# Kernel optimization log

Measured on AMD Instinct MI355X. Metric: run time of the kernel, lower is better.

## Reference

```python
import jax, jax.numpy as jnp
import numpy as np

NUM_ELECTRODES = 19
NUM_WINDOWS = 30
NUM_FREQS = 128
HEADS = 8
HID = 80
BATCH = 16
D_OUT = HEADS * HID  # 640


def _build_edge_index(num_nodes, num_windows):
    # spatiotemporal graph: dense intra-window blocks (incl. self-loops)
    # + bidirectional temporal edges between same electrode in adjacent windows
    srcs, dsts = [], []
    for w in range(num_windows):
        idx = np.arange(num_nodes) + w * num_nodes
        s, d = np.meshgrid(idx, idx, indexing='ij')
        srcs.append(s.ravel()); dsts.append(d.ravel())
    for w in range(num_windows - 1):
        a = np.arange(num_nodes) + w * num_nodes
        b = a + num_nodes
        srcs.append(a); dsts.append(b)
        srcs.append(b); dsts.append(a)
    return np.stack([np.concatenate(srcs), np.concatenate(dsts)]).astype(np.int32)


def setup_inputs() -> dict:
    key = jax.random.key(0)
    ks = jax.random.split(key, 12)
    f = NUM_FREQS
    x = jax.random.normal(ks[0], (BATCH, NUM_WINDOWS, NUM_FREQS, NUM_ELECTRODES), jnp.float32)
    s_in = 1.0 / np.sqrt(f)
    s_h = 1.0 / np.sqrt(D_OUT)
    Wl = jax.random.normal(ks[1], (D_OUT, f), jnp.float32) * s_in
    bl = jax.random.normal(ks[2], (D_OUT,), jnp.float32) * s_in
    Wr = jax.random.normal(ks[3], (D_OUT, f), jnp.float32) * s_in
    br = jax.random.normal(ks[4], (D_OUT,), jnp.float32) * s_in
    att = jax.random.normal(ks[5], (HEADS, HID), jnp.float32) * (1.0 / np.sqrt(HID))
    conv_bias = jax.random.normal(ks[6], (D_OUT,), jnp.float32) * 0.01
    Wpool = jax.random.normal(ks[7], (1, D_OUT), jnp.float32) * s_h
    bpool = jax.random.normal(ks[8], (1,), jnp.float32) * s_h
    Wfc = jax.random.normal(ks[9], (1, D_OUT), jnp.float32) * s_h
    bfc = jax.random.normal(ks[10], (1,), jnp.float32) * s_h
    edge_index = jnp.asarray(_build_edge_index(NUM_ELECTRODES, NUM_WINDOWS))
    return {"x": x, "edge_index": edge_index, "Wl": Wl, "bl": bl, "Wr": Wr, "br": br,
            "att": att, "conv_bias": conv_bias, "Wpool": Wpool, "bpool": bpool,
            "Wfc": Wfc, "bfc": bfc}


def reference(x, edge_index, Wl, bl, Wr, br, att, conv_bias, Wpool, bpool, Wfc, bfc):
    B, W, F, E19 = x.shape
    N = W * E19
    H, C = att.shape
    # (B, W, F, E) -> (B, W, E, F) -> (B, N, F)
    nodes = x.transpose(0, 1, 3, 2).reshape(B, N, F)
    src, dst = edge_index[0], edge_index[1]
    # GATv2: lin_l on source (messages), lin_r on target
    xl = (nodes @ Wl.T + bl).reshape(B, N, H, C)
    xr = (nodes @ Wr.T + br).reshape(B, N, H, C)
    msg = xl[:, src]                        # (B, E, H, C) source features
    key_feat = msg + xr[:, dst]             # (B, E, H, C)
    e = jnp.einsum('behc,hc->beh', jax.nn.leaky_relu(key_feat, 0.2), att)  # (B,E,H)

    def seg_softmax(e_b):  # (E, H), segment softmax over dst
        m = jax.ops.segment_max(e_b, dst, num_segments=N)
        ex = jnp.exp(e_b - m[dst])
        s = jax.ops.segment_sum(ex, dst, num_segments=N)
        return ex / (s[dst] + 1e-16)

    alpha = jax.vmap(seg_softmax)(e)        # (B, E, H)
    agg = jax.vmap(lambda m: jax.ops.segment_sum(m, dst, num_segments=N))(
        msg * alpha[..., None])             # (B, N, H, C)
    out = agg.reshape(B, N, H * C) + conv_bias
    out = jax.nn.elu(out)
    scores = out @ Wpool.T + bpool          # (B, N, 1)
    attn = jax.nn.softmax(scores, axis=1)
    pooled = (attn * out).sum(axis=1)       # (B, H*C)
    logits = pooled @ Wfc.T + bfc           # (B, 1)
    return logits.squeeze(1)
```

## Files before the change

kernel.cpp:

```cpp
#include <hip/hip_runtime.h>
#include <math.h>

#define B   16
#define NW  30
#define NE  19
#define NF  128
#define NH  8
#define NC  80
#define ND  640
#define NN  570
#define NROW (B*NN)

typedef _Float16 f16x2 __attribute__((ext_vector_type(2)));
typedef _Float16 f16x4 __attribute__((ext_vector_type(4)));
typedef _Float16 f16x8 __attribute__((ext_vector_type(8)));
typedef float    f32x16 __attribute__((ext_vector_type(16)));

#define WT_OFF   0
#define WT_SZ    (1280*128)
#define XL_OFF   (WT_OFF + WT_SZ)
#define XLR16_SZ (B*NN*ND/2)
#define XR_OFF   (XL_OFF + XLR16_SZ)
#define XT_OFF   (XR_OFF + XLR16_SZ)
#define SCP_OFF  (XT_OFF + 2*(NROW*NF/2))
#define SCP_SZ   (NH*B*NN)
#define QP_OFF   (SCP_OFF + SCP_SZ)

__global__ __launch_bounds__(256) void k0_prep(const float* __restrict__ Wl,
                                               const float* __restrict__ Wr,
                                               const float* __restrict__ x,
                                               _Float16* __restrict__ wph,
                                               _Float16* __restrict__ wpl,
                                               _Float16* __restrict__ xph,
                                               _Float16* __restrict__ xpl){
  int bx = blockIdx.x, t = threadIdx.x;
  if (bx < 160){
    int i = bx*256 + t;
    int dd = i >> 5, k = (i & 31) * 4;
    const float* srcp = (dd < 640) ? (Wl + dd*NF + k) : (Wr + (dd-640)*NF + k);
    float4 v = *(const float4*)srcp;
    _Float16 h0=(_Float16)v.x, h1=(_Float16)v.y, h2=(_Float16)v.z, h3=(_Float16)v.w;
    f16x4 hv = {h0, h1, h2, h3};
    f16x4 lv = {(_Float16)(v.x-(float)h0), (_Float16)(v.y-(float)h1),
                (_Float16)(v.z-(float)h2), (_Float16)(v.w-(float)h3)};
    int s = k >> 4, hh = (k >> 3) & 1, off = k & 7;
    size_t chunk = (((size_t)(dd >> 5)*8 + s)*64 + hh*32 + (dd & 31))*8 + off;
    *(f16x4*)(wph + chunk) = hv;
    *(f16x4*)(wpl + chunk) = lv;
    return;
  }
  int wb = bx - 160, w = wb % NW, b = wb / NW;
  __shared__ float ns[19*132];
  const float4* xs = (const float4*)(x + (size_t)((b*NW + w)*NF)*NE);
  for (int i = t; i < 608; i += 256){
    float4 v = xs[i];
    int idx = 4*i;
    float vv[4] = {v.x, v.y, v.z, v.w};
    #pragma unroll
    for (int k = 0; k < 4; ++k){
      int f = (idx + k) / NE, el = (idx + k) % NE;
      ns[el*132 + f] = vv[k];
    }
  }
  __syncthreads();
  for (int i = t; i < 608; i += 256){
    int el = i >> 5, k = (i & 31) * 4;
    float4 v = *(const float4*)&ns[el*132 + k];
    _Float16 h0=(_Float16)v.x, h1=(_Float16)v.y, h2=(_Float16)v.z, h3=(_Float16)v.w;
    f16x4 hv = {h0, h1, h2, h3};
    f16x4 lv = {(_Float16)(v.x-(float)h0), (_Float16)(v.y-(float)h1),
                (_Float16)(v.z-(float)h2), (_Float16)(v.w-(float)h3)};
    int n = (b*NW + w)*NE + el;
    int s = k >> 4, hh = (k >> 3) & 1, off = k & 7;
    size_t chunk = (((size_t)(n >> 5)*8 + s)*64 + hh*32 + (n & 31))*8 + off;
    *(f16x4*)(xph + chunk) = hv;
    *(f16x4*)(xpl + chunk) = lv;
  }
}

__global__ __launch_bounds__(256) void k1_gemm(const _Float16* __restrict__ xph,
                                               const _Float16* __restrict__ xpl,
                                               const _Float16* __restrict__ wph,
                                               const _Float16* __restrict__ wpl,
                                               const float* __restrict__ bl,
                                               const float* __restrict__ br,
                                               _Float16* __restrict__ xl,
                                               _Float16* __restrict__ xr){
  int t = threadIdx.x;
  int wave = t >> 6, lane = t & 63;
  int mt = blockIdx.x;
  int nt = blockIdx.y*4 + wave;

  __shared__ _Float16 ash[4096];
  __shared__ _Float16 asl[4096];
  {
    const f16x8* gh = (const f16x8*)(xph + (size_t)mt*4096);
    const f16x8* gl = (const f16x8*)(xpl + (size_t)mt*4096);
    f16x8* sh = (f16x8*)ash;
    f16x8* sl = (f16x8*)asl;
    #pragma unroll
    for (int c = 0; c < 2; ++c){
      sh[t + c*256] = gh[t + c*256];
      sl[t + c*256] = gl[t + c*256];
    }
  }
  __syncthreads();

  const f16x8* sah = (const f16x8*)ash + lane;
  const f16x8* sal = (const f16x8*)asl + lane;
  const f16x8* pbh = (const f16x8*)wph + (size_t)nt*8*64 + lane;
  const f16x8* pbl = (const f16x8*)wpl + (size_t)nt*8*64 + lane;

  f32x16 acc = {};
  #pragma unroll
  for (int s = 0; s < 8; ++s){
    f16x8 a_h = sah[s*64];
    f16x8 b_h = pbh[s*64];
    f16x8 a_l = sal[s*64];
    f16x8 b_l = pbl[s*64];
    acc = __builtin_amdgcn_mfma_f32_32x32x16_f16(a_h, b_h, acc, 0, 0, 0);
    acc = __builtin_amdgcn_mfma_f32_32x32x16_f16(a_l, b_h, acc, 0, 0, 0);
    acc = __builtin_amdgcn_mfma_f32_32x32x16_f16(a_h, b_l, acc, 0, 0, 0);
  }

  int bn = nt*32 + (lane & 31);
  float bias = (bn < 640) ? bl[bn] : br[bn - 640];
  _Float16* dstb = (bn < 640) ? xl : xr;
  int col = (bn < 640) ? bn : bn - 640;
  int rbase = mt*32 + 4*(lane >> 5);
  #pragma unroll
  for (int r = 0; r < 16; ++r){
    int node = rbase + (r & 3) + 8*(r >> 2);
    dstb[(size_t)node*ND + col] = (_Float16)(acc[r] + bias);
  }
}

__global__ __launch_bounds__(256, 4) void k2_gat(const _Float16* __restrict__ xl,
                                              const _Float16* __restrict__ xr,
                                              const float* __restrict__ att,
                                              const float* __restrict__ cb,
                                              const float* __restrict__ wpool,
                                              const float* __restrict__ wfc,
                                              float* __restrict__ scp,
                                              float* __restrict__ qp){
  int w = blockIdx.x, b = blockIdx.y, h = blockIdx.z, t = threadIdx.x;
  __shared__ _Float16 xl_s[57*88];
  __shared__ _Float16 xr_s[19*88];
  __shared__ _Float16 atth_s[80];
  __shared__ float cb_s[80], wp_s[80], wf_s[80];
  __shared__ float e_s[19*22];
  __shared__ float score_s[19], q_s[19];
  if (t < 19){ score_s[t] = 0.f; q_s[t] = 0.f; }
  const bool vp = (w > 0), vn = (w < NW-1);

  for (int i = t; i < 570; i += 256){
    int row = i / 10, c8 = i % 10;
    int node = -1;
    if (row < 19)        node = w*NE + row;
    else if (row < 38) { if (vp) node = (w-1)*NE + (row-19); }
    else               { if (vn) node = (w+1)*NE + (row-38); }
    if (node >= 0)
      *(f16x8*)&xl_s[row*88 + 8*c8] =
        *(const f16x8*)(xl + (size_t)(b*NN + node)*ND + h*80 + 8*c8);
  }
  for (int i = t; i < 190; i += 256){
    int row = i / 10, c8 = i % 10;
    int node = w*NE + row;
    *(f16x8*)&xr_s[row*88 + 8*c8] =
      *(const f16x8*)(xr + (size_t)(b*NN + node)*ND + h*80 + 8*c8);
  }
  if (t < 80){
    int a = t / 20, c4 = t % 20;
    if (a == 0){
      float4 v = *(const float4*)(att + h*80 + 4*c4);
      f16x4 hv = {(_Float16)v.x, (_Float16)v.y, (_Float16)v.z, (_Float16)v.w};
      *(f16x4*)&atth_s[4*c4] = hv;
    } else {
      const float* sp0 = (a == 1) ? cb + h*80 : (a == 2) ? wpool + h*80 : wfc + h*80;
      float*       dp  = (a == 1) ? cb_s      : (a == 2) ? wp_s        : wf_s;
      *(float4*)&dp[4*c4] = *(const float4*)(sp0 + 4*c4);
    }
  }
  __syncthreads();

  for (int eid = t; eid < 399; eid += 256){
    int s = eid / 19, dst = eid % 19;
    if ((s == 19 && !vp) || (s == 20 && !vn)) continue;
    int row = (s < 19) ? s : (s == 19 ? 19 + dst : 38 + dst);
    const f16x8* xlp = (const f16x8*)&xl_s[row*88];
    const f16x8* xrp = (const f16x8*)&xr_s[dst*88];
    const f16x8* ap  = (const f16x8*)atth_s;
    float acc = 0.f;
    #pragma unroll 2
    for (int c8 = 0; c8 < 10; ++c8){
      f16x8 z  = xlp[c8] + xrp[c8];
      f16x8 zs = z * (_Float16)0.2f;
      f16x8 zm = __builtin_elementwise_max(z, zs);
      f16x8 a8 = ap[c8];
#if __has_builtin(__builtin_amdgcn_fdot2)
      acc = __builtin_amdgcn_fdot2(__builtin_shufflevector(zm, zm, 0, 1),
                                   __builtin_shufflevector(a8, a8, 0, 1), acc, false);
      acc = __builtin_amdgcn_fdot2(__builtin_shufflevector(zm, zm, 2, 3),
                                   __builtin_shufflevector(a8, a8, 2, 3), acc, false);
      acc = __builtin_amdgcn_fdot2(__builtin_shufflevector(zm, zm, 4, 5),
                                   __builtin_shufflevector(a8, a8, 4, 5), acc, false);
      acc = __builtin_amdgcn_fdot2(__builtin_shufflevector(zm, zm, 6, 7),
                                   __builtin_shufflevector(a8, a8, 6, 7), acc, false);
#else
      #pragma unroll
      for (int j = 0; j < 8; ++j)
        acc = fmaf((float)zm[j], (float)a8[j], acc);
#endif
    }
    e_s[dst*22 + s] = acc;
  }
  __syncthreads();

  if (t < 19){
    float* base = &e_s[t*22];
    float m = -1e30f;
    for (int s = 0; s < 21; ++s){
      if ((s == 19 && !vp) || (s == 20 && !vn)) continue;
      m = fmaxf(m, base[s]);
    }
    float sum = 0.f;
    for (int s = 0; s < 21; ++s){
      if ((s == 19 && !vp) || (s == 20 && !vn)) continue;
      float ex = __expf(base[s] - m); base[s] = ex; sum += ex;
    }
    base[21] = 1.f / (sum + 1e-16f);
  }
  __syncthreads();

  if (t < 190){
    int dst = t / 10, c0 = (t % 10) * 8;
    float acc[8];
    #pragma unroll
    for (int j = 0; j < 8; ++j) acc[j] = 0.f;
    for (int s = 0; s < 21; ++s){
      if ((s == 19 && !vp) || (s == 20 && !vn)) continue;
      int row = (s < 19) ? s : (s == 19 ? 19 + dst : 38 + dst);
      float al = e_s[dst*22 + s];
      f16x8 v = *(const f16x8*)&xl_s[row*88 + c0];
      #pragma unroll
      for (int j = 0; j < 8; ++j) acc[j] = fmaf(al, (float)v[j], acc[j]);
    }
    float inv = e_s[dst*22 + 21];
    float sp = 0.f, fq = 0.f;
    #pragma unroll
    for (int k = 0; k < 8; ++k){
      float v = fmaf(inv, acc[k], cb_s[c0 + k]);
      v = (v > 0.f) ? v : (__expf(v) - 1.f);
      sp += v * wp_s[c0 + k];
      fq += v * wf_s[c0 + k];
    }
    atomicAdd(&score_s[dst], sp);
    atomicAdd(&q_s[dst], fq);
  }
  __syncthreads();
  if (t < 19){
    size_t o = ((size_t)h*B + b)*NN + w*NE + t;
    scp[o] = score_s[t];
    qp[o]  = q_s[t];
  }
}

__global__ __launch_bounds__(256) void k3_final(const float* __restrict__ scp,
                                                const float* __restrict__ qp,
                                                const float* __restrict__ bpool,
                                                const float* __restrict__ bfc,
                                                float* __restrict__ out){
  int b = blockIdx.x, t = threadIdx.x;
  __shared__ float ss[NN], qq[NN];
  __shared__ float red[4], rs[4], rq[4];
  float bp = bpool[0];
  for (int i = t; i < NN; i += 256){
    float v = bp, q = 0.f;
    #pragma unroll
    for (int h = 0; h < NH; ++h){
      v += scp[((size_t)h*B + b)*NN + i];
      q += qp [((size_t)h*B + b)*NN + i];
    }
    ss[i] = v; qq[i] = q;
  }
  __syncthreads();
  float m = -1e30f;
  for (int i = t; i < NN; i += 256) m = fmaxf(m, ss[i]);
  for (int off = 32; off > 0; off >>= 1) m = fmaxf(m, __shfl_down(m, off));
  int wid = t >> 6, lane = t & 63;
  if (lane == 0) red[wid] = m;
  __syncthreads();
  if (t == 0) red[0] = fmaxf(fmaxf(red[0], red[1]), fmaxf(red[2], red[3]));
  __syncthreads();
  m = red[0];
  float s = 0.f, qs = 0.f;
  for (int i = t; i < NN; i += 256){
    float e = __expf(ss[i] - m);
    s += e; qs += e * qq[i];
  }
  for (int off = 32; off > 0; off >>= 1){
    s  += __shfl_down(s, off);
    qs += __shfl_down(qs, off);
  }
  if (lane == 0){ rs[wid] = s; rq[wid] = qs; }
  __syncthreads();
  if (t == 0){
    float S = rs[0] + rs[1] + rs[2] + rs[3];
    float Q = rq[0] + rq[1] + rq[2] + rq[3];
    out[b] = Q / (S + 1e-16f) + bfc[0];
  }
}

extern "C" void kernel_launch(void* const* d_in, const int* in_sizes, int n_in,
                              void* d_out, int out_size, void* d_ws, size_t ws_size,
                              hipStream_t stream){
  const float* x     = (const float*)d_in[0];
  const float* Wl    = (const float*)d_in[2];
  const float* bl    = (const float*)d_in[3];
  const float* Wr    = (const float*)d_in[4];
  const float* br    = (const float*)d_in[5];
  const float* att   = (const float*)d_in[6];
  const float* cb    = (const float*)d_in[7];
  const float* wpool = (const float*)d_in[8];
  const float* bpool = (const float*)d_in[9];
  const float* wfc   = (const float*)d_in[10];
  const float* bfc   = (const float*)d_in[11];

  float* ws      = (float*)d_ws;
  _Float16* wph  = (_Float16*)(ws + WT_OFF);
  _Float16* wpl  = wph + 1280*NF;
  _Float16* xlb  = (_Float16*)(ws + XL_OFF);
  _Float16* xrb  = (_Float16*)(ws + XR_OFF);
  _Float16* xph  = (_Float16*)(ws + XT_OFF);
  _Float16* xpl  = xph + (size_t)NROW*NF;
  float* scp     = ws + SCP_OFF;
  float* qp      = ws + QP_OFF;

  k0_prep  <<<640, 256, 0, stream>>>(Wl, Wr, x, wph, wpl, xph, xpl);
  k1_gemm  <<<dim3(285, 10), 256, 0, stream>>>(xph, xpl, wph, wpl, bl, br, xlb, xrb);
  k2_gat   <<<dim3(NW, B, NH), 256, 0, stream>>>(xlb, xrb, att, cb, wpool, wfc, scp, qp);
  k3_final <<<B, 256, 0, stream>>>(scp, qp, bpool, bfc, (float*)d_out);
}
```

Measured before the change: 136.7 us.

## Widen GEMM and GAT blocks to reuse A tiles and process four heads per block

```diff
diff --git a/kernel.cpp b/kernel.cpp
--- a/kernel.cpp
+++ b/kernel.cpp
@@ -25,6 +25,23 @@
 #define SCP_OFF  (XT_OFF + 2*(NROW*NF/2))
 #define SCP_SZ   (NH*B*NN)
 #define QP_OFF   (SCP_OFF + SCP_SZ)
+
+__device__ __forceinline__ float dot8(f16x8 zm, f16x8 a8, float acc){
+#if __has_builtin(__builtin_amdgcn_fdot2)
+  acc = __builtin_amdgcn_fdot2(__builtin_shufflevector(zm, zm, 0, 1),
+                               __builtin_shufflevector(a8, a8, 0, 1), acc, false);
+  acc = __builtin_amdgcn_fdot2(__builtin_shufflevector(zm, zm, 2, 3),
+                               __builtin_shufflevector(a8, a8, 2, 3), acc, false);
+  acc = __builtin_amdgcn_fdot2(__builtin_shufflevector(zm, zm, 4, 5),
+                               __builtin_shufflevector(a8, a8, 4, 5), acc, false);
+  acc = __builtin_amdgcn_fdot2(__builtin_shufflevector(zm, zm, 6, 7),
+                               __builtin_shufflevector(a8, a8, 6, 7), acc, false);
+#else
+  #pragma unroll
+  for (int j = 0; j < 8; ++j) acc = fmaf((float)zm[j], (float)a8[j], acc);
+#endif
+  return acc;
+}
 
 __global__ __launch_bounds__(256) void k0_prep(const float* __restrict__ Wl,
                                                const float* __restrict__ Wr,
@@ -88,54 +105,75 @@
                                                _Float16* __restrict__ xr){
   int t = threadIdx.x;
   int wave = t >> 6, lane = t & 63;
-  int mt = blockIdx.x;
-  int nt = blockIdx.y*4 + wave;
+  int mt = blockIdx.x, y = blockIdx.y;
 
   __shared__ _Float16 ash[4096];
   __shared__ _Float16 asl[4096];
   {
     const f16x8* gh = (const f16x8*)(xph + (size_t)mt*4096);
     const f16x8* gl = (const f16x8*)(xpl + (size_t)mt*4096);
-    f16x8* sh = (f16x8*)ash;
-    f16x8* sl = (f16x8*)asl;
     #pragma unroll
     for (int c = 0; c < 2; ++c){
-      sh[t + c*256] = gh[t + c*256];
-      sl[t + c*256] = gl[t + c*256];
-    }
-  }
-  __syncthreads();
-
-  const f16x8* sah = (const f16x8*)ash + lane;
-  const f16x8* sal = (const f16x8*)asl + lane;
-  const f16x8* pbh = (const f16x8*)wph + (size_t)nt*8*64 + lane;
-  const f16x8* pbl = (const f16x8*)wpl + (size_t)nt*8*64 + lane;
-
-  f32x16 acc = {};
+      ((f16x8*)ash)[t + c*256] = gh[t + c*256];
+      ((f16x8*)asl)[t + c*256] = gl[t + c*256];
+    }
+  }
+  __syncthreads();
+
+  f16x8 Ah[8], Al[8];
   #pragma unroll
   for (int s = 0; s < 8; ++s){
-    f16x8 a_h = sah[s*64];
-    f16x8 b_h = pbh[s*64];
-    f16x8 a_l = sal[s*64];
-    f16x8 b_l = pbl[s*64];
-    acc = __builtin_amdgcn_mfma_f32_32x32x16_f16(a_h, b_h, acc, 0, 0, 0);
-    acc = __builtin_amdgcn_mfma_f32_32x32x16_f16(a_l, b_h, acc, 0, 0, 0);
-    acc = __builtin_amdgcn_mfma_f32_32x32x16_f16(a_h, b_l, acc, 0, 0, 0);
-  }
-
-  int bn = nt*32 + (lane & 31);
-  float bias = (bn < 640) ? bl[bn] : br[bn - 640];
-  _Float16* dstb = (bn < 640) ? xl : xr;
-  int col = (bn < 640) ? bn : bn - 640;
-  int rbase = mt*32 + 4*(lane >> 5);
+    Ah[s] = ((const f16x8*)ash)[s*64 + lane];
+    Al[s] = ((const f16x8*)asl)[s*64 + lane];
+  }
+
+  const f16x8* bh0 = (const f16x8*)wph + lane;
+  const f16x8* bl0 = (const f16x8*)wpl + lane;
+  int nt0 = y*20 + wave;
+
+  f16x8 Bh[2][8], Bl[2][8];
   #pragma unroll
-  for (int r = 0; r < 16; ++r){
-    int node = rbase + (r & 3) + 8*(r >> 2);
-    dstb[(size_t)node*ND + col] = (_Float16)(acc[r] + bias);
-  }
-}
-
-__global__ __launch_bounds__(256, 4) void k2_gat(const _Float16* __restrict__ xl,
+  for (int s = 0; s < 8; ++s){
+    Bh[0][s] = bh0[(size_t)nt0*512 + s*64];
+    Bl[0][s] = bl0[(size_t)nt0*512 + s*64];
+  }
+
+  _Float16* dstb = y ? xr : xl;
+  const float* bias = y ? br : bl;
+  int node = mt*32 + (lane & 31);
+  _Float16* drow = dstb + (size_t)node*ND;
+  int cl4 = 4*(lane >> 5);
+
+  #pragma unroll
+  for (int i = 0; i < 5; ++i){
+    if (i < 4){
+      int ntn = nt0 + 4*(i+1);
+      #pragma unroll
+      for (int s = 0; s < 8; ++s){
+        Bh[(i+1)&1][s] = bh0[(size_t)ntn*512 + s*64];
+        Bl[(i+1)&1][s] = bl0[(size_t)ntn*512 + s*64];
+      }
+    }
+    f32x16 acc = {};
+    #pragma unroll
+    for (int s = 0; s < 8; ++s){
+      acc = __builtin_amdgcn_mfma_f32_32x32x16_f16(Bh[i&1][s], Ah[s], acc, 0, 0, 0);
+      acc = __builtin_amdgcn_mfma_f32_32x32x16_f16(Bh[i&1][s], Al[s], acc, 0, 0, 0);
+      acc = __builtin_amdgcn_mfma_f32_32x32x16_f16(Bl[i&1][s], Ah[s], acc, 0, 0, 0);
+    }
+    int colb = wave*32 + 128*i + cl4;
+    #pragma unroll
+    for (int g = 0; g < 4; ++g){
+      int ch = colb + 8*g;
+      float4 bb = *(const float4*)(bias + ch);
+      f16x4 o = {(_Float16)(acc[4*g+0] + bb.x), (_Float16)(acc[4*g+1] + bb.y),
+                 (_Float16)(acc[4*g+2] + bb.z), (_Float16)(acc[4*g+3] + bb.w)};
+      *(f16x4*)(drow + ch) = o;
+    }
+  }
+}
+
+__global__ __launch_bounds__(256) void k2_gat(const _Float16* __restrict__ xl,
                                               const _Float16* __restrict__ xr,
                                               const float* __restrict__ att,
                                               const float* __restrict__ cb,
@@ -143,81 +181,62 @@
                                               const float* __restrict__ wfc,
                                               float* __restrict__ scp,
                                               float* __restrict__ qp){
-  int w = blockIdx.x, b = blockIdx.y, h = blockIdx.z, t = threadIdx.x;
-  __shared__ _Float16 xl_s[57*88];
-  __shared__ _Float16 xr_s[19*88];
-  __shared__ _Float16 atth_s[80];
-  __shared__ float cb_s[80], wp_s[80], wf_s[80];
-  __shared__ float e_s[19*22];
-  __shared__ float score_s[19], q_s[19];
-  if (t < 19){ score_s[t] = 0.f; q_s[t] = 0.f; }
+  int w = blockIdx.x, b = blockIdx.y, z = blockIdx.z, t = threadIdx.x;
+  int h0 = z*4;
+  __shared__ _Float16 xl4[57*328];
+  __shared__ _Float16 xr4[19*328];
+  __shared__ _Float16 att4[320];
+  __shared__ float cb4[320], wp4[320], wf4[320];
+  __shared__ float e4[4*19*22];
+  __shared__ float sc4[76], qq4[76];
+  if (t < 76){ sc4[t] = 0.f; qq4[t] = 0.f; }
   const bool vp = (w > 0), vn = (w < NW-1);
 
-  for (int i = t; i < 570; i += 256){
-    int row = i / 10, c8 = i % 10;
+  for (int i = t; i < 2280; i += 256){
+    int r = i / 40, c = i % 40;
     int node = -1;
-    if (row < 19)        node = w*NE + row;
-    else if (row < 38) { if (vp) node = (w-1)*NE + (row-19); }
-    else               { if (vn) node = (w+1)*NE + (row-38); }
+    if (r < 19)        node = w*NE + r;
+    else if (r < 38) { if (vp) node = (w-1)*NE + (r-19); }
+    else             { if (vn) node = (w+1)*NE + (r-38); }
     if (node >= 0)
-      *(f16x8*)&xl_s[row*88 + 8*c8] =
-        *(const f16x8*)(xl + (size_t)(b*NN + node)*ND + h*80 + 8*c8);
-  }
-  for (int i = t; i < 190; i += 256){
-    int row = i / 10, c8 = i % 10;
-    int node = w*NE + row;
-    *(f16x8*)&xr_s[row*88 + 8*c8] =
-      *(const f16x8*)(xr + (size_t)(b*NN + node)*ND + h*80 + 8*c8);
-  }
-  if (t < 80){
-    int a = t / 20, c4 = t % 20;
-    if (a == 0){
-      float4 v = *(const float4*)(att + h*80 + 4*c4);
-      f16x4 hv = {(_Float16)v.x, (_Float16)v.y, (_Float16)v.z, (_Float16)v.w};
-      *(f16x4*)&atth_s[4*c4] = hv;
-    } else {
-      const float* sp0 = (a == 1) ? cb + h*80 : (a == 2) ? wpool + h*80 : wfc + h*80;
-      float*       dp  = (a == 1) ? cb_s      : (a == 2) ? wp_s        : wf_s;
-      *(float4*)&dp[4*c4] = *(const float4*)(sp0 + 4*c4);
-    }
-  }
-  __syncthreads();
-
-  for (int eid = t; eid < 399; eid += 256){
-    int s = eid / 19, dst = eid % 19;
+      *(f16x8*)&xl4[r*328 + c*8] =
+        *(const f16x8*)(xl + (size_t)(b*NN + node)*ND + h0*80 + c*8);
+  }
+  for (int i = t; i < 760; i += 256){
+    int r = i / 40, c = i % 40;
+    int node = w*NE + r;
+    *(f16x8*)&xr4[r*328 + c*8] =
+      *(const f16x8*)(xr + (size_t)(b*NN + node)*ND + h0*80 + c*8);
+  }
+  for (int i = t; i < 320; i += 256){
+    att4[i] = (_Float16)att[h0*80 + i];
+    cb4[i]  = cb[h0*80 + i];
+    wp4[i]  = wpool[h0*80 + i];
+    wf4[i]  = wfc[h0*80 + i];
+  }
+  __syncthreads();
+
+  for (int eid = t; eid < 1596; eid += 256){
+    int s = eid / 76, r2 = eid - s*76, dst = r2 >> 2, hh = r2 & 3;
     if ((s == 19 && !vp) || (s == 20 && !vn)) continue;
     int row = (s < 19) ? s : (s == 19 ? 19 + dst : 38 + dst);
-    const f16x8* xlp = (const f16x8*)&xl_s[row*88];
-    const f16x8* xrp = (const f16x8*)&xr_s[dst*88];
-    const f16x8* ap  = (const f16x8*)atth_s;
+    const f16x8* xlp = (const f16x8*)&xl4[row*328 + hh*80];
+    const f16x8* xrp = (const f16x8*)&xr4[dst*328 + hh*80];
+    const f16x8* ap  = (const f16x8*)&att4[hh*80];
     float acc = 0.f;
     #pragma unroll 2
     for (int c8 = 0; c8 < 10; ++c8){
-      f16x8 z  = xlp[c8] + xrp[c8];
-      f16x8 zs = z * (_Float16)0.2f;
-      f16x8 zm = __builtin_elementwise_max(z, zs);
-      f16x8 a8 = ap[c8];
-#if __has_builtin(__builtin_amdgcn_fdot2)
-      acc = __builtin_amdgcn_fdot2(__builtin_shufflevector(zm, zm, 0, 1),
-                                   __builtin_shufflevector(a8, a8, 0, 1), acc, false);
-      acc = __builtin_amdgcn_fdot2(__builtin_shufflevector(zm, zm, 2, 3),
-                                   __builtin_shufflevector(a8, a8, 2, 3), acc, false);
-      acc = __builtin_amdgcn_fdot2(__builtin_shufflevector(zm, zm, 4, 5),
-                                   __builtin_shufflevector(a8, a8, 4, 5), acc, false);
-      acc = __builtin_amdgcn_fdot2(__builtin_shufflevector(zm, zm, 6, 7),
-                                   __builtin_shufflevector(a8, a8, 6, 7), acc, false);
-#else
-      #pragma unroll
-      for (int j = 0; j < 8; ++j)
-        acc = fmaf((float)zm[j], (float)a8[j], acc);
-#endif
-    }
-    e_s[dst*22 + s] = acc;
-  }
-  __syncthreads();
-
-  if (t < 19){
-    float* base = &e_s[t*22];
+      f16x8 zv = xlp[c8] + xrp[c8];
+      f16x8 zm = __builtin_elementwise_max(zv, zv * (_Float16)0.2f);
+      acc = dot8(zm, ap[c8], acc);
+    }
+    e4[hh*418 + dst*22 + s] = acc;
+  }
+  __syncthreads();
+
+  if (t < 76){
+    int hh = t / 19, dst = t % 19;
+    float* base = &e4[hh*418 + dst*22];
     float m = -1e30f;
     for (int s = 0; s < 21; ++s){
       if ((s == 19 && !vp) || (s == 20 && !vn)) continue;
@@ -232,36 +251,37 @@
   }
   __syncthreads();
 
-  if (t < 190){
-    int dst = t / 10, c0 = (t % 10) * 8;
+  for (int idx = t; idx < 760; idx += 256){
+    int hh = idx / 190, rr = idx - hh*190, dst = rr / 10, c0 = (rr % 10) * 8;
     float acc[8];
     #pragma unroll
     for (int j = 0; j < 8; ++j) acc[j] = 0.f;
     for (int s = 0; s < 21; ++s){
       if ((s == 19 && !vp) || (s == 20 && !vn)) continue;
       int row = (s < 19) ? s : (s == 19 ? 19 + dst : 38 + dst);
-      float al = e_s[dst*22 + s];
-      f16x8 v = *(const f16x8*)&xl_s[row*88 + c0];
+      float al = e4[hh*418 + dst*22 + s];
+      f16x8 v = *(const f16x8*)&xl4[row*328 + hh*80 + c0];
       #pragma unroll
       for (int j = 0; j < 8; ++j) acc[j] = fmaf(al, (float)v[j], acc[j]);
     }
-    float inv = e_s[dst*22 + 21];
+    float inv = e4[hh*418 + dst*22 + 21];
     float sp = 0.f, fq = 0.f;
     #pragma unroll
     for (int k = 0; k < 8; ++k){
-      float v = fmaf(inv, acc[k], cb_s[c0 + k]);
+      float v = fmaf(inv, acc[k], cb4[hh*80 + c0 + k]);
       v = (v > 0.f) ? v : (__expf(v) - 1.f);
-      sp += v * wp_s[c0 + k];
-      fq += v * wf_s[c0 + k];
-    }
-    atomicAdd(&score_s[dst], sp);
-    atomicAdd(&q_s[dst], fq);
-  }
-  __syncthreads();
-  if (t < 19){
-    size_t o = ((size_t)h*B + b)*NN + w*NE + t;
-    scp[o] = score_s[t];
-    qp[o]  = q_s[t];
+      sp += v * wp4[hh*80 + c0 + k];
+      fq += v * wf4[hh*80 + c0 + k];
+    }
+    atomicAdd(&sc4[hh*19 + dst], sp);
+    atomicAdd(&qq4[hh*19 + dst], fq);
+  }
+  __syncthreads();
+  if (t < 76){
+    int hh = t / 19, dst = t % 19;
+    size_t o = ((size_t)(h0 + hh)*B + b)*NN + w*NE + dst;
+    scp[o] = sc4[t];
+    qp[o]  = qq4[t];
   }
 }
 
@@ -337,7 +357,7 @@
   float* qp      = ws + QP_OFF;
 
   k0_prep  <<<640, 256, 0, stream>>>(Wl, Wr, x, wph, wpl, xph, xpl);
-  k1_gemm  <<<dim3(285, 10), 256, 0, stream>>>(xph, xpl, wph, wpl, bl, br, xlb, xrb);
-  k2_gat   <<<dim3(NW, B, NH), 256, 0, stream>>>(xlb, xrb, att, cb, wpool, wfc, scp, qp);
+  k1_gemm  <<<dim3(285, 2), 256, 0, stream>>>(xph, xpl, wph, wpl, bl, br, xlb, xrb);
+  k2_gat   <<<dim3(NW, B, 2), 256, 0, stream>>>(xlb, xrb, att, cb, wpool, wfc, scp, qp);
   k3_final <<<B, 256, 0, stream>>>(scp, qp, bpool, bfc, (float*)d_out);
 }
```

Measured after the change: 162.5 us. +18.9%, slower.

## Store xl/xr head-major and bulk-copy contiguous neighbor rows into LDS

Applied to the files above, without the earlier changes.

```diff
diff --git a/kernel.cpp b/kernel.cpp
--- a/kernel.cpp
+++ b/kernel.cpp
@@ -25,6 +25,33 @@
 #define SCP_OFF  (XT_OFF + 2*(NROW*NF/2))
 #define SCP_SZ   (NH*B*NN)
 #define QP_OFF   (SCP_OFF + SCP_SZ)
+
+__device__ __forceinline__ void load_lds16(const void* g, void* l){
+#if __has_builtin(__builtin_amdgcn_global_load_lds)
+  __builtin_amdgcn_global_load_lds(
+      (const __attribute__((address_space(1))) unsigned int*)g,
+      (__attribute__((address_space(3))) unsigned int*)l, 16, 0, 0);
+#else
+  *(f16x8*)l = *(const f16x8*)g;
+#endif
+}
+
+__device__ __forceinline__ float dot8(f16x8 zm, f16x8 a8, float acc){
+#if __has_builtin(__builtin_amdgcn_fdot2)
+  acc = __builtin_amdgcn_fdot2(__builtin_shufflevector(zm, zm, 0, 1),
+                               __builtin_shufflevector(a8, a8, 0, 1), acc, false);
+  acc = __builtin_amdgcn_fdot2(__builtin_shufflevector(zm, zm, 2, 3),
+                               __builtin_shufflevector(a8, a8, 2, 3), acc, false);
+  acc = __builtin_amdgcn_fdot2(__builtin_shufflevector(zm, zm, 4, 5),
+                               __builtin_shufflevector(a8, a8, 4, 5), acc, false);
+  acc = __builtin_amdgcn_fdot2(__builtin_shufflevector(zm, zm, 6, 7),
+                               __builtin_shufflevector(a8, a8, 6, 7), acc, false);
+#else
+  #pragma unroll
+  for (int j = 0; j < 8; ++j) acc = fmaf((float)zm[j], (float)a8[j], acc);
+#endif
+  return acc;
+}
 
 __global__ __launch_bounds__(256) void k0_prep(const float* __restrict__ Wl,
                                                const float* __restrict__ Wr,
@@ -96,12 +123,10 @@
   {
     const f16x8* gh = (const f16x8*)(xph + (size_t)mt*4096);
     const f16x8* gl = (const f16x8*)(xpl + (size_t)mt*4096);
-    f16x8* sh = (f16x8*)ash;
-    f16x8* sl = (f16x8*)asl;
     #pragma unroll
     for (int c = 0; c < 2; ++c){
-      sh[t + c*256] = gh[t + c*256];
-      sl[t + c*256] = gl[t + c*256];
+      ((f16x8*)ash)[t + c*256] = gh[t + c*256];
+      ((f16x8*)asl)[t + c*256] = gl[t + c*256];
     }
   }
   __syncthreads();
@@ -124,18 +149,21 @@
   }
 
   int bn = nt*32 + (lane & 31);
-  float bias = (bn < 640) ? bl[bn] : br[bn - 640];
-  _Float16* dstb = (bn < 640) ? xl : xr;
-  int col = (bn < 640) ? bn : bn - 640;
+  bool isl = bn < 640;
+  int col = isl ? bn : bn - 640;
+  float bias = isl ? bl[bn] : br[col];
+  _Float16* dstb = isl ? xl : xr;
+  int h = col / 80, c = col % 80;
   int rbase = mt*32 + 4*(lane >> 5);
   #pragma unroll
   for (int r = 0; r < 16; ++r){
-    int node = rbase + (r & 3) + 8*(r >> 2);
-    dstb[(size_t)node*ND + col] = (_Float16)(acc[r] + bias);
-  }
-}
-
-__global__ __launch_bounds__(256, 4) void k2_gat(const _Float16* __restrict__ xl,
+    int row = rbase + (r & 3) + 8*(r >> 2);
+    int bb = row / 570, n = row - bb*570;
+    dstb[((size_t)(h*B + bb)*NN + n)*80 + c] = (_Float16)(acc[r] + bias);
+  }
+}
+
+__global__ __launch_bounds__(256) void k2_gat(const _Float16* __restrict__ xl,
                                               const _Float16* __restrict__ xr,
                                               const float* __restrict__ att,
                                               const float* __restrict__ cb,
@@ -143,8 +171,13 @@
                                               const float* __restrict__ wfc,
                                               float* __restrict__ scp,
                                               float* __restrict__ qp){
-  int w = blockIdx.x, b = blockIdx.y, h = blockIdx.z, t = threadIdx.x;
-  __shared__ _Float16 xl_s[57*88];
+  int t = threadIdx.x;
+  int wg = blockIdx.x + NW*(blockIdx.y + B*blockIdx.z);
+  int idx = (wg & 7)*480 + (wg >> 3);
+  int w = idx % NW, rem = idx / NW;
+  int b = rem % B, h = rem / B;
+
+  __shared__ __attribute__((aligned(16))) _Float16 xl_s[57*80];
   __shared__ _Float16 xr_s[19*88];
   __shared__ _Float16 atth_s[80];
   __shared__ float cb_s[80], wp_s[80], wf_s[80];
@@ -152,22 +185,17 @@
   __shared__ float score_s[19], q_s[19];
   if (t < 19){ score_s[t] = 0.f; q_s[t] = 0.f; }
   const bool vp = (w > 0), vn = (w < NW-1);
-
-  for (int i = t; i < 570; i += 256){
-    int row = i / 10, c8 = i % 10;
-    int node = -1;
-    if (row < 19)        node = w*NE + row;
-    else if (row < 38) { if (vp) node = (w-1)*NE + (row-19); }
-    else               { if (vn) node = (w+1)*NE + (row-38); }
-    if (node >= 0)
-      *(f16x8*)&xl_s[row*88 + 8*c8] =
-        *(const f16x8*)(xl + (size_t)(b*NN + node)*ND + h*80 + 8*c8);
-  }
+  const int own0 = vp ? 19 : 0;
+  const int nrows = 19 + (vp ? 19 : 0) + (vn ? 19 : 0);
+  const int lo = (vp ? w-1 : w)*NE;
+
+  const _Float16* xsrc = xl + ((size_t)(h*B + b)*NN + lo)*80;
+  for (int i = t; i < nrows*10; i += 256)
+    load_lds16(xsrc + i*8, &xl_s[i*8]);
+  const _Float16* rsrc = xr + ((size_t)(h*B + b)*NN + (size_t)w*NE)*80;
   for (int i = t; i < 190; i += 256){
     int row = i / 10, c8 = i % 10;
-    int node = w*NE + row;
-    *(f16x8*)&xr_s[row*88 + 8*c8] =
-      *(const f16x8*)(xr + (size_t)(b*NN + node)*ND + h*80 + 8*c8);
+    *(f16x8*)&xr_s[row*88 + 8*c8] = *(const f16x8*)(rsrc + row*80 + 8*c8);
   }
   if (t < 80){
     int a = t / 20, c4 = t % 20;
@@ -186,31 +214,16 @@
   for (int eid = t; eid < 399; eid += 256){
     int s = eid / 19, dst = eid % 19;
     if ((s == 19 && !vp) || (s == 20 && !vn)) continue;
-    int row = (s < 19) ? s : (s == 19 ? 19 + dst : 38 + dst);
-    const f16x8* xlp = (const f16x8*)&xl_s[row*88];
+    int row = (s < 19) ? own0 + s : (s == 19 ? dst : own0 + 19 + dst);
+    const f16x8* xlp = (const f16x8*)&xl_s[row*80];
     const f16x8* xrp = (const f16x8*)&xr_s[dst*88];
     const f16x8* ap  = (const f16x8*)atth_s;
     float acc = 0.f;
     #pragma unroll 2
     for (int c8 = 0; c8 < 10; ++c8){
       f16x8 z  = xlp[c8] + xrp[c8];
-      f16x8 zs = z * (_Float16)0.2f;
-      f16x8 zm = __builtin_elementwise_max(z, zs);
-      f16x8 a8 = ap[c8];
-#if __has_builtin(__builtin_amdgcn_fdot2)
-      acc = __builtin_amdgcn_fdot2(__builtin_shufflevector(zm, zm, 0, 1),
-                                   __builtin_shufflevector(a8, a8, 0, 1), acc, false);
-      acc = __builtin_amdgcn_fdot2(__builtin_shufflevector(zm, zm, 2, 3),
-                                   __builtin_shufflevector(a8, a8, 2, 3), acc, false);
-      acc = __builtin_amdgcn_fdot2(__builtin_shufflevector(zm, zm, 4, 5),
-                                   __builtin_shufflevector(a8, a8, 4, 5), acc, false);
-      acc = __builtin_amdgcn_fdot2(__builtin_shufflevector(zm, zm, 6, 7),
-                                   __builtin_shufflevector(a8, a8, 6, 7), acc, false);
-#else
-      #pragma unroll
-      for (int j = 0; j < 8; ++j)
-        acc = fmaf((float)zm[j], (float)a8[j], acc);
-#endif
+      f16x8 zm = __builtin_elementwise_max(z, z * (_Float16)0.2f);
+      acc = dot8(zm, ap[c8], acc);
     }
     e_s[dst*22 + s] = acc;
   }
@@ -239,9 +252,9 @@
     for (int j = 0; j < 8; ++j) acc[j] = 0.f;
     for (int s = 0; s < 21; ++s){
       if ((s == 19 && !vp) || (s == 20 && !vn)) continue;
-      int row = (s < 19) ? s : (s == 19 ? 19 + dst : 38 + dst);
+      int row = (s < 19) ? own0 + s : (s == 19 ? dst : own0 + 19 + dst);
       float al = e_s[dst*22 + s];
-      f16x8 v = *(const f16x8*)&xl_s[row*88 + c0];
+      f16x8 v = *(const f16x8*)&xl_s[row*80 + c0];
       #pragma unroll
       for (int j = 0; j < 8; ++j) acc[j] = fmaf(al, (float)v[j], acc[j]);
     }
@@ -259,7 +272,7 @@
   }
   __syncthreads();
   if (t < 19){
-    size_t o = ((size_t)h*B + b)*NN + w*NE + t;
+    size_t o = ((size_t)h*B + b)*NN + (size_t)w*NE + t;
     scp[o] = score_s[t];
     qp[o]  = q_s[t];
   }
```

Result: slower. 142.5 us (+4.3%).
